# Kernel optimization log

Measured on AMD Instinct MI355X. Metric: run time of the kernel, lower is better.

## Reference

```python
import jax, jax.numpy as jnp
import numpy as np

N_NODES = 100000
N_EDGES = 1600000
D_IN = 64
D_HID = 64
D_ACT = 16


def gcn_conv(x, W, b, src, dst, n_nodes):
    """PyG-style GCNConv: D^-1/2 (A+I) D^-1/2 (x @ W) + b."""
    h = x @ W  # [N, out]
    ones = jnp.ones(src.shape[0], dtype=x.dtype)
    # degree with self-loops (in-degree + 1)
    deg = jax.ops.segment_sum(ones, dst, num_segments=n_nodes) + 1.0
    dinv = jax.lax.rsqrt(deg)  # [N]
    coef = dinv[src] * dinv[dst]  # [E]
    agg = jax.ops.segment_sum(h[src] * coef[:, None], dst, num_segments=n_nodes)
    agg = agg + h * (dinv * dinv)[:, None]  # self-loop term
    return agg + b


def setup_inputs() -> dict:
    key = jax.random.key(0)
    ks = jax.random.split(key, 6)
    x = jax.random.normal(ks[0], (N_NODES, D_IN), dtype=jnp.float32)
    edge_index = jax.random.randint(ks[1], (2, N_EDGES), 0, N_NODES, dtype=jnp.int64)
    s1 = 1.0 / np.sqrt(D_IN)
    s2 = 1.0 / np.sqrt(D_HID)
    W1 = jax.random.normal(ks[2], (D_IN, D_HID), dtype=jnp.float32) * s1
    b1 = jnp.zeros((D_HID,), dtype=jnp.float32)
    W2 = jax.random.normal(ks[3], (D_HID, D_HID), dtype=jnp.float32) * s2
    b2 = jnp.zeros((D_HID,), dtype=jnp.float32)
    Wfc = jax.random.normal(ks[4], (D_HID, D_ACT), dtype=jnp.float32) * s2
    bfc = jnp.zeros((D_ACT,), dtype=jnp.float32)
    return {"x": x, "edge_index": edge_index, "W1": W1, "b1": b1,
            "W2": W2, "b2": b2, "Wfc": Wfc, "bfc": bfc}


def reference(x, edge_index, W1, b1, W2, b2, Wfc, bfc):
    src, dst = edge_index[0], edge_index[1]
    n = x.shape[0]
    h = jax.nn.relu(gcn_conv(x, W1, b1, src, dst, n))
    h = jax.nn.relu(gcn_conv(h, W2, b2, src, dst, n))
    q_values = h @ Wfc + bfc
    return q_values
```

## Files before the change

kernel.cpp:

```cpp
#include <hip/hip_runtime.h>

#define NN 100000
#define NE 1600000
#define NCAP 64
#define NB2 782
#define NBP2 1024
#define CAPG 384
#define CHUNK 2048
#define NCHUNK 782

typedef __attribute__((ext_vector_type(8))) short short8;
typedef __attribute__((ext_vector_type(4))) float f32x4;

static __device__ __forceinline__ unsigned short f2bf(float f) {
    unsigned u = __float_as_uint(f);
    u += 0x7fffu + ((u >> 16) & 1u);
    return (unsigned short)(u >> 16);
}
static __device__ __forceinline__ float bflo(unsigned u) { return __uint_as_float(u << 16); }
static __device__ __forceinline__ float bfhi(unsigned u) { return __uint_as_float(u & 0xffff0000u); }

static __device__ __forceinline__ short8 as_s8(uint4 u) {
    union { uint4 u4; short8 s8; } x; x.u4 = u; return x.s8;
}
static __device__ __forceinline__ f32x4 mfma16(short8 a, short8 b, f32x4 c) {
    return __builtin_amdgcn_mfma_f32_16x16x32_bf16(a, b, c, 0, 0, 0);
}

static __device__ __forceinline__ void split8(float4 a, float4 b, short8& hi8, short8& lo8) {
    float vv[8] = {a.x, a.y, a.z, a.w, b.x, b.y, b.z, b.w};
    unsigned h[8], l[8];
    #pragma unroll
    for (int j = 0; j < 8; ++j) {
        h[j] = f2bf(vv[j]);
        l[j] = f2bf(vv[j] - bflo(h[j]));
    }
    uint4 uh, ul;
    uh.x = h[0] | (h[1] << 16); uh.y = h[2] | (h[3] << 16);
    uh.z = h[4] | (h[5] << 16); uh.w = h[6] | (h[7] << 16);
    ul.x = l[0] | (l[1] << 16); ul.y = l[2] | (l[3] << 16);
    ul.z = l[4] | (l[5] << 16); ul.w = l[6] | (l[7] << 16);
    hi8 = as_s8(uh); lo8 = as_s8(ul);
}

__global__ __launch_bounds__(256) void bin_edges(const int* __restrict__ src,
                                                 const int* __restrict__ dst,
                                                 int* __restrict__ gcur,
                                                 int* __restrict__ pairs) {
    __shared__ int lcnt[NBP2];
    __shared__ int lnext[NBP2];
    int t = threadIdx.x;
    int grp = blockIdx.x & 7;
    #pragma unroll
    for (int i = 0; i < 4; ++i) lcnt[t + 256 * i] = 0;
    __syncthreads();
    int base = blockIdx.x * CHUNK;
    int sr[8], dr[8];
    #pragma unroll
    for (int i = 0; i < 8; ++i) {
        int e = base + t + 256 * i;
        bool v = e < NE;
        sr[i] = v ? src[e] : 0;
        dr[i] = v ? dst[e] : -1;
        if (v) atomicAdd(&lcnt[dr[i] >> 7], 1);
    }
    __syncthreads();
    #pragma unroll
    for (int i = 0; i < 4; ++i) {
        int b = t + 256 * i;
        int v = lcnt[b];
        if (v) lnext[b] = ((grp << 10) + b) * CAPG + atomicAdd(&gcur[(grp << 10) + b], v);
    }
    __syncthreads();
    #pragma unroll
    for (int i = 0; i < 8; ++i) {
        if (dr[i] >= 0) {
            int p = atomicAdd(&lnext[dr[i] >> 7], 1);
            pairs[p] = sr[i] | ((dr[i] & 127) << 17);
        }
    }
}

__global__ __launch_bounds__(256) void slab_place(const int* __restrict__ pairs,
                                                  const int* __restrict__ gcur,
                                                  int* __restrict__ esrc,
                                                  int* __restrict__ cnt,
                                                  float* __restrict__ dinv) {
    __shared__ int lc[128];
    int b = blockIdx.x;
    int t = threadIdx.x;
    if (t < 128) lc[t] = 0;
    __syncthreads();
    #pragma unroll
    for (int g = 0; g < 8; ++g) {
        int rid = (g << 10) + b;
        int e0 = rid * CAPG;
        int n = min(gcur[rid], CAPG);
        for (int i = t; i < n; i += 256) {
            int w = pairs[e0 + i];
            int li = w >> 17;
            int p = atomicAdd(&lc[li], 1);
            if (p < NCAP - 1) esrc[(((b << 7) + li) << 6) + p] = w & 0x1FFFF;
        }
    }
    __syncthreads();
    if (t < 128) {
        int node = (b << 7) + t;
        if (node < NN) {
            int c = lc[t];
            int cc = min(c, NCAP - 1);
            esrc[(node << 6) + cc] = node;
            cnt[node] = cc + 1;
            dinv[node] = rsqrtf((float)c + 1.0f);
        }
    }
}

__global__ void wpack(const float* __restrict__ W1, const float* __restrict__ W2,
                      uint4* __restrict__ P, int* __restrict__ gcur) {
    int tid = blockIdx.x * blockDim.x + threadIdx.x;
    if (tid >= 1024) return;
    #pragma unroll
    for (int k = 0; k < 8; ++k) gcur[tid + 1024 * k] = 0;
    int w = tid >> 9;
    int f = tid & 511;
    int c = f >> 7;
    int t = (f >> 6) & 1;
    int lane = f & 63;
    const float* W = w ? W2 : W1;
    int k0 = t * 32 + (lane >> 4) * 8;
    int n  = c * 16 + (lane & 15);
    unsigned sh[8], sl[8];
    #pragma unroll
    for (int j = 0; j < 8; ++j) {
        float v = W[(k0 + j) * 64 + n];
        sh[j] = f2bf(v);
        sl[j] = f2bf(v - bflo(sh[j]));
    }
    uint4 ph, pl;
    ph.x = sh[0] | (sh[1] << 16); ph.y = sh[2] | (sh[3] << 16);
    ph.z = sh[4] | (sh[5] << 16); ph.w = sh[6] | (sh[7] << 16);
    pl.x = sl[0] | (sl[1] << 16); pl.y = sl[2] | (sl[3] << 16);
    pl.z = sl[4] | (sl[5] << 16); pl.w = sl[6] | (sl[7] << 16);
    P[w * 1024 + f]       = ph;
    P[w * 1024 + 512 + f] = pl;
}

__global__ __launch_bounds__(256) void gemm1_mfma(const float* __restrict__ X,
                                                  const uint4* __restrict__ WP,
                                                  const float* __restrict__ dinv,
                                                  uint4* __restrict__ G4) {
    __shared__ __align__(16) unsigned short Ls[4][16][64];
    int wave = threadIdx.x >> 6, lane = threadIdx.x & 63;
    int tile = blockIdx.x * 4 + wave;
    bool active = tile < (NN / 16);
    int node0 = (active ? tile : 0) * 16;
    int r = lane & 15, g = lane >> 4;

    const float* xr = X + (size_t)(node0 + r) * 64 + g * 8;
    float4 x0a = *(const float4*)(xr);
    float4 x0b = *(const float4*)(xr + 4);
    float4 x1a = *(const float4*)(xr + 32);
    float4 x1b = *(const float4*)(xr + 36);
    short8 ah0, al0, ah1, al1;
    split8(x0a, x0b, ah0, al0);
    split8(x1a, x1b, ah1, al1);

    f32x4 acc[4];
    #pragma unroll
    for (int c = 0; c < 4; ++c) acc[c] = (f32x4){0.f, 0.f, 0.f, 0.f};
    #pragma unroll
    for (int c = 0; c < 4; ++c) {
        short8 bh0 = as_s8(WP[(c * 2 + 0) * 64 + lane]);
        short8 bl0 = as_s8(WP[512 + (c * 2 + 0) * 64 + lane]);
        short8 bh1 = as_s8(WP[(c * 2 + 1) * 64 + lane]);
        short8 bl1 = as_s8(WP[512 + (c * 2 + 1) * 64 + lane]);
        acc[c] = mfma16(ah0, bh0, acc[c]);
        acc[c] = mfma16(al0, bh0, acc[c]);
        acc[c] = mfma16(ah0, bl0, acc[c]);
        acc[c] = mfma16(ah1, bh1, acc[c]);
        acc[c] = mfma16(al1, bh1, acc[c]);
        acc[c] = mfma16(ah1, bl1, acc[c]);
    }
    float dd[4];
    #pragma unroll
    for (int rr = 0; rr < 4; ++rr) dd[rr] = dinv[node0 + g * 4 + rr];
    #pragma unroll
    for (int c = 0; c < 4; ++c) {
        #pragma unroll
        for (int rr = 0; rr < 4; ++rr)
            Ls[wave][g * 4 + rr][c * 16 + r] = f2bf(acc[c][rr] * dd[rr]);
    }
    __syncthreads();
    if (active) {
        #pragma unroll
        for (int i = 0; i < 2; ++i) {
            int idx = lane + i * 64;
            int row = idx >> 3, u = idx & 7;
            G4[(size_t)(node0 + row) * 8 + u] = *(const uint4*)&Ls[wave][row][u * 8];
        }
    }
}

__global__ __launch_bounds__(256) void gemm2_mfma(const uint4* __restrict__ X4,
                                                  const uint4* __restrict__ WP,
                                                  const float* __restrict__ dinv,
                                                  uint4* __restrict__ G4) {
    __shared__ __align__(16) unsigned short Ls[4][16][64];
    int wave = threadIdx.x >> 6, lane = threadIdx.x & 63;
    int tile = blockIdx.x * 4 + wave;
    bool active = tile < (NN / 16);
    int node0 = (active ? tile : 0) * 16;
    int r = lane & 15, g = lane >> 4;

    short8 a0 = as_s8(X4[(size_t)(node0 + r) * 8 + g]);
    short8 a1 = as_s8(X4[(size_t)(node0 + r) * 8 + 4 + g]);

    f32x4 acc[4];
    #pragma unroll
    for (int c = 0; c < 4; ++c) acc[c] = (f32x4){0.f, 0.f, 0.f, 0.f};
    #pragma unroll
    for (int c = 0; c < 4; ++c) {
        short8 bh0 = as_s8(WP[(c * 2 + 0) * 64 + lane]);
        short8 bl0 = as_s8(WP[512 + (c * 2 + 0) * 64 + lane]);
        short8 bh1 = as_s8(WP[(c * 2 + 1) * 64 + lane]);
        short8 bl1 = as_s8(WP[512 + (c * 2 + 1) * 64 + lane]);
        acc[c] = mfma16(a0, bh0, acc[c]);
        acc[c] = mfma16(a0, bl0, acc[c]);
        acc[c] = mfma16(a1, bh1, acc[c]);
        acc[c] = mfma16(a1, bl1, acc[c]);
    }
    float dd[4];
    #pragma unroll
    for (int rr = 0; rr < 4; ++rr) dd[rr] = dinv[node0 + g * 4 + rr];
    #pragma unroll
    for (int c = 0; c < 4; ++c) {
        #pragma unroll
        for (int rr = 0; rr < 4; ++rr)
            Ls[wave][g * 4 + rr][c * 16 + r] = f2bf(acc[c][rr] * dd[rr]);
    }
    __syncthreads();
    if (active) {
        #pragma unroll
        for (int i = 0; i < 2; ++i) {
            int idx = lane + i * 64;
            int row = idx >> 3, u = idx & 7;
            G4[(size_t)(node0 + row) * 8 + u] = *(const uint4*)&Ls[wave][row][u * 8];
        }
    }
}

#define ACC8(u) do { \
    a0 += bflo((u).x); a1 += bfhi((u).x); a2 += bflo((u).y); a3 += bfhi((u).y); \
    a4 += bflo((u).z); a5 += bfhi((u).z); a6 += bflo((u).w); a7 += bfhi(u.w); } while (0)

#define GATHER_CORE(node)                                                     \
    int j0 = (node) << 6;                                                     \
    int e1 = j0 + cnt[node];                                                  \
    float a0 = 0.f, a1 = 0.f, a2 = 0.f, a3 = 0.f,                             \
          a4 = 0.f, a5 = 0.f, a6 = 0.f, a7 = 0.f;                             \
    int j = j0 + e;                                                           \
    for (; j + 8 < e1; j += 16) {                                             \
        int s0 = esrc[j], s1 = esrc[j + 8];                                   \
        uint4 u0 = G4[s0 * 8 + m];                                            \
        uint4 u1 = G4[s1 * 8 + m];                                            \
        ACC8(u0); ACC8(u1);                                                   \
    }                                                                         \
    for (; j < e1; j += 8) {                                                  \
        uint4 u = G4[esrc[j] * 8 + m];                                        \
        ACC8(u);                                                              \
    }                                                                         \
    a0 += __shfl_xor(a0, 8);  a1 += __shfl_xor(a1, 8);                        \
    a2 += __shfl_xor(a2, 8);  a3 += __shfl_xor(a3, 8);                        \
    a4 += __shfl_xor(a4, 8);  a5 += __shfl_xor(a5, 8);                        \
    a6 += __shfl_xor(a6, 8);  a7 += __shfl_xor(a7, 8);                        \
    a0 += __shfl_xor(a0, 16); a1 += __shfl_xor(a1, 16);                       \
    a2 += __shfl_xor(a2, 16); a3 += __shfl_xor(a3, 16);                       \
    a4 += __shfl_xor(a4, 16); a5 += __shfl_xor(a5, 16);                       \
    a6 += __shfl_xor(a6, 16); a7 += __shfl_xor(a7, 16);                       \
    a0 += __shfl_xor(a0, 32); a1 += __shfl_xor(a1, 32);                       \
    a2 += __shfl_xor(a2, 32); a3 += __shfl_xor(a3, 32);                       \
    a4 += __shfl_xor(a4, 32); a5 += __shfl_xor(a5, 32);                       \
    a6 += __shfl_xor(a6, 32); a7 += __shfl_xor(a7, 32);

__global__ __launch_bounds__(256) void gather_bf16(
        const int* __restrict__ cnt, const int* __restrict__ esrc,
        const float* __restrict__ dinv, const uint4* __restrict__ G4,
        const float* __restrict__ b, uint4* __restrict__ outH) {
    int node = blockIdx.x * 4 + (threadIdx.x >> 6);
    int lane = threadIdx.x & 63;
    int e = lane >> 3, m = lane & 7;
    GATHER_CORE(node)
    if (e == 0) {
        float dd = dinv[node];
        float4 b0 = ((const float4*)b)[2 * m];
        float4 b1v = ((const float4*)b)[2 * m + 1];
        float h0 = fmaxf(fmaf(a0, dd, b0.x), 0.f);
        float h1 = fmaxf(fmaf(a1, dd, b0.y), 0.f);
        float h2 = fmaxf(fmaf(a2, dd, b0.z), 0.f);
        float h3 = fmaxf(fmaf(a3, dd, b0.w), 0.f);
        float h4 = fmaxf(fmaf(a4, dd, b1v.x), 0.f);
        float h5 = fmaxf(fmaf(a5, dd, b1v.y), 0.f);
        float h6 = fmaxf(fmaf(a6, dd, b1v.z), 0.f);
        float h7 = fmaxf(fmaf(a7, dd, b1v.w), 0.f);
        uint4 pk;
        pk.x = (unsigned)f2bf(h0) | ((unsigned)f2bf(h1) << 16);
        pk.y = (unsigned)f2bf(h2) | ((unsigned)f2bf(h3) << 16);
        pk.z = (unsigned)f2bf(h4) | ((unsigned)f2bf(h5) << 16);
        pk.w = (unsigned)f2bf(h6) | ((unsigned)f2bf(h7) << 16);
        outH[(size_t)node * 8 + m] = pk;
    }
}

__global__ __launch_bounds__(256) void gather_fc(
        const int* __restrict__ cnt, const int* __restrict__ esrc,
        const float* __restrict__ dinv, const uint4* __restrict__ G4,
        const float* __restrict__ b2, const float* __restrict__ Wfc,
        const float* __restrict__ bfc, float* __restrict__ out) {
    int node = blockIdx.x * 4 + (threadIdx.x >> 6);
    int lane = threadIdx.x & 63;
    int e = lane >> 3, m = lane & 7;
    int q = lane >> 4, c = lane & 15;
    float Wreg[16];
    #pragma unroll
    for (int i = 0; i < 16; ++i) Wreg[i] = Wfc[(q * 16 + i) * 16 + c];
    GATHER_CORE(node)
    float dd = dinv[node];
    float4 b0 = ((const float4*)b2)[2 * m];
    float4 b1v = ((const float4*)b2)[2 * m + 1];
    a0 = fmaxf(fmaf(a0, dd, b0.x), 0.f);
    a1 = fmaxf(fmaf(a1, dd, b0.y), 0.f);
    a2 = fmaxf(fmaf(a2, dd, b0.z), 0.f);
    a3 = fmaxf(fmaf(a3, dd, b0.w), 0.f);
    a4 = fmaxf(fmaf(a4, dd, b1v.x), 0.f);
    a5 = fmaxf(fmaf(a5, dd, b1v.y), 0.f);
    a6 = fmaxf(fmaf(a6, dd, b1v.z), 0.f);
    a7 = fmaxf(fmaf(a7, dd, b1v.w), 0.f);
    int sl0 = 2 * q, sl1 = 2 * q + 1;
    float acc = 0.f;
    acc = fmaf(__shfl(a0, sl0), Wreg[0], acc);
    acc = fmaf(__shfl(a1, sl0), Wreg[1], acc);
    acc = fmaf(__shfl(a2, sl0), Wreg[2], acc);
    acc = fmaf(__shfl(a3, sl0), Wreg[3], acc);
    acc = fmaf(__shfl(a4, sl0), Wreg[4], acc);
    acc = fmaf(__shfl(a5, sl0), Wreg[5], acc);
    acc = fmaf(__shfl(a6, sl0), Wreg[6], acc);
    acc = fmaf(__shfl(a7, sl0), Wreg[7], acc);
    acc = fmaf(__shfl(a0, sl1), Wreg[8], acc);
    acc = fmaf(__shfl(a1, sl1), Wreg[9], acc);
    acc = fmaf(__shfl(a2, sl1), Wreg[10], acc);
    acc = fmaf(__shfl(a3, sl1), Wreg[11], acc);
    acc = fmaf(__shfl(a4, sl1), Wreg[12], acc);
    acc = fmaf(__shfl(a5, sl1), Wreg[13], acc);
    acc = fmaf(__shfl(a6, sl1), Wreg[14], acc);
    acc = fmaf(__shfl(a7, sl1), Wreg[15], acc);
    acc += __shfl_xor(acc, 16);
    acc += __shfl_xor(acc, 32);
    if (lane < 16) out[node * 16 + c] = acc + bfc[c];
}

extern "C" void kernel_launch(void* const* d_in, const int* in_sizes, int n_in,
                              void* d_out, int out_size, void* d_ws, size_t ws_size,
                              hipStream_t stream) {
    const float* x   = (const float*)d_in[0];
    const int*   ei  = (const int*)d_in[1];
    const float* W1  = (const float*)d_in[2];
    const float* b1  = (const float*)d_in[3];
    const float* W2  = (const float*)d_in[4];
    const float* b2  = (const float*)d_in[5];
    const float* Wfc = (const float*)d_in[6];
    const float* bfc = (const float*)d_in[7];
    float* out = (float*)d_out;

    const int* src = ei;
    const int* dst = ei + NE;

    int*      gcur  = (int*)d_ws;
    int*      cnt   = gcur + 8192;
    float*    dinvp = (float*)(cnt + NN);
    int*      esrc  = (int*)(dinvp + NN);
    unsigned* G     = (unsigned*)(esrc + (size_t)NN * NCAP);
    uint4*    bufB  = (uint4*)(G + (size_t)NN * 32);
    uint4*    WPK   = (uint4*)((unsigned*)bufB + (size_t)NN * 32);
    int*      pairs = (int*)bufB;

    wpack<<<4, 256, 0, stream>>>(W1, W2, WPK, gcur);
    bin_edges<<<NCHUNK, 256, 0, stream>>>(src, dst, gcur, pairs);
    slab_place<<<NB2, 256, 0, stream>>>(pairs, gcur, esrc, cnt, dinvp);

    gemm1_mfma<<<(NN / 16 + 3) / 4, 256, 0, stream>>>(x, WPK, dinvp, (uint4*)G);
    gather_bf16<<<NN / 4, 256, 0, stream>>>(cnt, esrc, dinvp, (const uint4*)G, b1, bufB);

    gemm2_mfma<<<(NN / 16 + 3) / 4, 256, 0, stream>>>(bufB, WPK + 1024, dinvp, (uint4*)G);
    gather_fc<<<NN / 4, 256, 0, stream>>>(cnt, esrc, dinvp, (const uint4*)G, b2, Wfc, bfc, out);
}
```

Baseline: 228.5 us.

## Fuse second-layer GEMM into first gather kernel via per-node MFMA

Removes the separate gemm2 kernel. Each wave that aggregates one node in the first gather now also multiplies the resulting hidden row by W2 using MFMA, with the row placed in lane r==0 of a 16-row tile and the other rows zeroed. It then writes the dinv-scaled bf16 G2 row directly. This saves a kernel launch and a full write and read of the intermediate hidden buffer. In exchange each wave issues 16 MFMAs and reloads the W2 fragments for a single useful row, so 15/16 of the matrix work is wasted.

```diff
diff --git a/kernel.cpp b/kernel.cpp
--- a/kernel.cpp
+++ b/kernel.cpp
@@ -202,57 +202,9 @@
     }
 }
 
-__global__ __launch_bounds__(256) void gemm2_mfma(const uint4* __restrict__ X4,
-                                                  const uint4* __restrict__ WP,
-                                                  const float* __restrict__ dinv,
-                                                  uint4* __restrict__ G4) {
-    __shared__ __align__(16) unsigned short Ls[4][16][64];
-    int wave = threadIdx.x >> 6, lane = threadIdx.x & 63;
-    int tile = blockIdx.x * 4 + wave;
-    bool active = tile < (NN / 16);
-    int node0 = (active ? tile : 0) * 16;
-    int r = lane & 15, g = lane >> 4;
-
-    short8 a0 = as_s8(X4[(size_t)(node0 + r) * 8 + g]);
-    short8 a1 = as_s8(X4[(size_t)(node0 + r) * 8 + 4 + g]);
-
-    f32x4 acc[4];
-    #pragma unroll
-    for (int c = 0; c < 4; ++c) acc[c] = (f32x4){0.f, 0.f, 0.f, 0.f};
-    #pragma unroll
-    for (int c = 0; c < 4; ++c) {
-        short8 bh0 = as_s8(WP[(c * 2 + 0) * 64 + lane]);
-        short8 bl0 = as_s8(WP[512 + (c * 2 + 0) * 64 + lane]);
-        short8 bh1 = as_s8(WP[(c * 2 + 1) * 64 + lane]);
-        short8 bl1 = as_s8(WP[512 + (c * 2 + 1) * 64 + lane]);
-        acc[c] = mfma16(a0, bh0, acc[c]);
-        acc[c] = mfma16(a0, bl0, acc[c]);
-        acc[c] = mfma16(a1, bh1, acc[c]);
-        acc[c] = mfma16(a1, bl1, acc[c]);
-    }
-    float dd[4];
-    #pragma unroll
-    for (int rr = 0; rr < 4; ++rr) dd[rr] = dinv[node0 + g * 4 + rr];
-    #pragma unroll
-    for (int c = 0; c < 4; ++c) {
-        #pragma unroll
-        for (int rr = 0; rr < 4; ++rr)
-            Ls[wave][g * 4 + rr][c * 16 + r] = f2bf(acc[c][rr] * dd[rr]);
-    }
-    __syncthreads();
-    if (active) {
-        #pragma unroll
-        for (int i = 0; i < 2; ++i) {
-            int idx = lane + i * 64;
-            int row = idx >> 3, u = idx & 7;
-            G4[(size_t)(node0 + row) * 8 + u] = *(const uint4*)&Ls[wave][row][u * 8];
-        }
-    }
-}
-
 #define ACC8(u) do { \
     a0 += bflo((u).x); a1 += bfhi((u).x); a2 += bflo((u).y); a3 += bfhi((u).y); \
-    a4 += bflo((u).z); a5 += bfhi((u).z); a6 += bflo((u).w); a7 += bfhi(u.w); } while (0)
+    a4 += bflo((u).z); a5 += bfhi((u).z); a6 += bflo((u).w); a7 += bfhi((u).w); } while (0)
 
 #define GATHER_CORE(node)                                                     \
     int j0 = (node) << 6;                                                     \
@@ -283,32 +235,76 @@
     a4 += __shfl_xor(a4, 32); a5 += __shfl_xor(a5, 32);                       \
     a6 += __shfl_xor(a6, 32); a7 += __shfl_xor(a7, 32);
 
-__global__ __launch_bounds__(256) void gather_bf16(
+__global__ __launch_bounds__(256) void gather_g2(
         const int* __restrict__ cnt, const int* __restrict__ esrc,
         const float* __restrict__ dinv, const uint4* __restrict__ G4,
-        const float* __restrict__ b, uint4* __restrict__ outH) {
-    int node = blockIdx.x * 4 + (threadIdx.x >> 6);
+        const float* __restrict__ b, const uint4* __restrict__ WP2,
+        uint4* __restrict__ G2) {
+    __shared__ float Ls[4][64];
+    int wave = threadIdx.x >> 6;
+    int node = blockIdx.x * 4 + wave;
     int lane = threadIdx.x & 63;
     int e = lane >> 3, m = lane & 7;
     GATHER_CORE(node)
-    if (e == 0) {
-        float dd = dinv[node];
-        float4 b0 = ((const float4*)b)[2 * m];
-        float4 b1v = ((const float4*)b)[2 * m + 1];
-        float h0 = fmaxf(fmaf(a0, dd, b0.x), 0.f);
-        float h1 = fmaxf(fmaf(a1, dd, b0.y), 0.f);
-        float h2 = fmaxf(fmaf(a2, dd, b0.z), 0.f);
-        float h3 = fmaxf(fmaf(a3, dd, b0.w), 0.f);
-        float h4 = fmaxf(fmaf(a4, dd, b1v.x), 0.f);
-        float h5 = fmaxf(fmaf(a5, dd, b1v.y), 0.f);
-        float h6 = fmaxf(fmaf(a6, dd, b1v.z), 0.f);
-        float h7 = fmaxf(fmaf(a7, dd, b1v.w), 0.f);
+    float dd = dinv[node];
+    float4 b0 = ((const float4*)b)[2 * m];
+    float4 b1v = ((const float4*)b)[2 * m + 1];
+    float h0 = fmaxf(fmaf(a0, dd, b0.x), 0.f);
+    float h1 = fmaxf(fmaf(a1, dd, b0.y), 0.f);
+    float h2 = fmaxf(fmaf(a2, dd, b0.z), 0.f);
+    float h3 = fmaxf(fmaf(a3, dd, b0.w), 0.f);
+    float h4 = fmaxf(fmaf(a4, dd, b1v.x), 0.f);
+    float h5 = fmaxf(fmaf(a5, dd, b1v.y), 0.f);
+    float h6 = fmaxf(fmaf(a6, dd, b1v.z), 0.f);
+    float h7 = fmaxf(fmaf(a7, dd, b1v.w), 0.f);
+    int r = lane & 15, g = lane >> 4;
+    bool live = (r == 0);
+    float t00 = __shfl(h0, g),     t01 = __shfl(h1, g),     t02 = __shfl(h2, g),     t03 = __shfl(h3, g);
+    float t04 = __shfl(h4, g),     t05 = __shfl(h5, g),     t06 = __shfl(h6, g),     t07 = __shfl(h7, g);
+    float t10 = __shfl(h0, 4 + g), t11 = __shfl(h1, 4 + g), t12 = __shfl(h2, 4 + g), t13 = __shfl(h3, 4 + g);
+    float t14 = __shfl(h4, 4 + g), t15 = __shfl(h5, 4 + g), t16 = __shfl(h6, 4 + g), t17 = __shfl(h7, 4 + g);
+    uint4 pk0, pk1;
+    if (live) {
+        pk0.x = (unsigned)f2bf(t00) | ((unsigned)f2bf(t01) << 16);
+        pk0.y = (unsigned)f2bf(t02) | ((unsigned)f2bf(t03) << 16);
+        pk0.z = (unsigned)f2bf(t04) | ((unsigned)f2bf(t05) << 16);
+        pk0.w = (unsigned)f2bf(t06) | ((unsigned)f2bf(t07) << 16);
+        pk1.x = (unsigned)f2bf(t10) | ((unsigned)f2bf(t11) << 16);
+        pk1.y = (unsigned)f2bf(t12) | ((unsigned)f2bf(t13) << 16);
+        pk1.z = (unsigned)f2bf(t14) | ((unsigned)f2bf(t15) << 16);
+        pk1.w = (unsigned)f2bf(t16) | ((unsigned)f2bf(t17) << 16);
+    } else {
+        pk0 = make_uint4(0, 0, 0, 0);
+        pk1 = make_uint4(0, 0, 0, 0);
+    }
+    short8 pa0 = as_s8(pk0), pa1 = as_s8(pk1);
+    float g2v[4];
+    #pragma unroll
+    for (int c = 0; c < 4; ++c) {
+        short8 bh0 = as_s8(WP2[(c * 2 + 0) * 64 + lane]);
+        short8 bl0 = as_s8(WP2[512 + (c * 2 + 0) * 64 + lane]);
+        short8 bh1 = as_s8(WP2[(c * 2 + 1) * 64 + lane]);
+        short8 bl1 = as_s8(WP2[512 + (c * 2 + 1) * 64 + lane]);
+        f32x4 t4 = (f32x4){0.f, 0.f, 0.f, 0.f};
+        t4 = mfma16(pa0, bh0, t4);
+        t4 = mfma16(pa0, bl0, t4);
+        t4 = mfma16(pa1, bh1, t4);
+        t4 = mfma16(pa1, bl1, t4);
+        g2v[c] = t4[0];
+    }
+    if (lane < 16) {
+        #pragma unroll
+        for (int c = 0; c < 4; ++c) Ls[wave][c * 16 + lane] = g2v[c] * dd;
+    }
+    if (lane < 8) {
+        float4 va = *(const float4*)&Ls[wave][8 * lane];
+        float4 vb = *(const float4*)&Ls[wave][8 * lane + 4];
         uint4 pk;
-        pk.x = (unsigned)f2bf(h0) | ((unsigned)f2bf(h1) << 16);
-        pk.y = (unsigned)f2bf(h2) | ((unsigned)f2bf(h3) << 16);
-        pk.z = (unsigned)f2bf(h4) | ((unsigned)f2bf(h5) << 16);
-        pk.w = (unsigned)f2bf(h6) | ((unsigned)f2bf(h7) << 16);
-        outH[(size_t)node * 8 + m] = pk;
+        pk.x = (unsigned)f2bf(va.x) | ((unsigned)f2bf(va.y) << 16);
+        pk.y = (unsigned)f2bf(va.z) | ((unsigned)f2bf(va.w) << 16);
+        pk.z = (unsigned)f2bf(vb.x) | ((unsigned)f2bf(vb.y) << 16);
+        pk.w = (unsigned)f2bf(vb.z) | ((unsigned)f2bf(vb.w) << 16);
+        G2[(size_t)node * 8 + lane] = pk;
     }
 }
 
@@ -380,17 +376,17 @@
     float*    dinvp = (float*)(cnt + NN);
     int*      esrc  = (int*)(dinvp + NN);
     unsigned* G     = (unsigned*)(esrc + (size_t)NN * NCAP);
-    uint4*    bufB  = (uint4*)(G + (size_t)NN * 32);
-    uint4*    WPK   = (uint4*)((unsigned*)bufB + (size_t)NN * 32);
-    int*      pairs = (int*)bufB;
+    uint4*    G2    = (uint4*)(G + (size_t)NN * 32);
+    uint4*    WPK   = (uint4*)((unsigned*)G2 + (size_t)NN * 32);
+    int*      pairs = (int*)G2;
 
     wpack<<<4, 256, 0, stream>>>(W1, W2, WPK, gcur);
     bin_edges<<<NCHUNK, 256, 0, stream>>>(src, dst, gcur, pairs);
     slab_place<<<NB2, 256, 0, stream>>>(pairs, gcur, esrc, cnt, dinvp);
 
     gemm1_mfma<<<(NN / 16 + 3) / 4, 256, 0, stream>>>(x, WPK, dinvp, (uint4*)G);
-    gather_bf16<<<NN / 4, 256, 0, stream>>>(cnt, esrc, dinvp, (const uint4*)G, b1, bufB);
-
-    gemm2_mfma<<<(NN / 16 + 3) / 4, 256, 0, stream>>>(bufB, WPK + 1024, dinvp, (uint4*)G);
-    gather_fc<<<NN / 4, 256, 0, stream>>>(cnt, esrc, dinvp, (const uint4*)G, b2, Wfc, bfc, out);
-}
+    gather_g2<<<NN / 4, 256, 0, stream>>>(cnt, esrc, dinvp, (const uint4*)G, b1,
+                                          WPK + 1024, G2);
+
+    gather_fc<<<NN / 4, 256, 0, stream>>>(cnt, esrc, dinvp, (const uint4*)G2, b2, Wfc, bfc, out);
+}
```

After: 251.8 us. 10.2% more time.

## Fuse edge slab placement with first-layer GEMM into one kernel

Applied to the files above, without the earlier changes.

Merges slab_place and gemm1_mfma into a single kernel. Each block places edges for its 128 nodes, computes dinv into shared memory, then runs the MFMA GEMM for those same 128 nodes. This removes one kernel launch and the global dinv reload. The pair reads are also widened to int4 vector loads, and the __syncthreads before the per-wave store in gemm2 is dropped because each wave only reads its own LDS tile. In exchange, the GEMM work now depends on per-block atomic placement finishing, which may serialize the two phases within a block.

```diff
diff --git a/kernel.cpp b/kernel.cpp
--- a/kernel.cpp
+++ b/kernel.cpp
@@ -81,12 +81,17 @@
     }
 }
 
-__global__ __launch_bounds__(256) void slab_place(const int* __restrict__ pairs,
+__global__ __launch_bounds__(256) void slab_gemm1(const int* __restrict__ pairs,
                                                   const int* __restrict__ gcur,
+                                                  const float* __restrict__ X,
+                                                  const uint4* __restrict__ WP,
                                                   int* __restrict__ esrc,
                                                   int* __restrict__ cnt,
-                                                  float* __restrict__ dinv) {
+                                                  float* __restrict__ dinv,
+                                                  uint4* __restrict__ G4) {
     __shared__ int lc[128];
+    __shared__ float ldv[128];
+    __shared__ __align__(16) unsigned short Ls[4][16][64];
     int b = blockIdx.x;
     int t = threadIdx.x;
     if (t < 128) lc[t] = 0;
@@ -96,11 +101,18 @@
         int rid = (g << 10) + b;
         int e0 = rid * CAPG;
         int n = min(gcur[rid], CAPG);
-        for (int i = t; i < n; i += 256) {
-            int w = pairs[e0 + i];
-            int li = w >> 17;
-            int p = atomicAdd(&lc[li], 1);
-            if (p < NCAP - 1) esrc[(((b << 7) + li) << 6) + p] = w & 0x1FFFF;
+        for (int i0 = t * 4; i0 < n; i0 += 1024) {
+            int4 w4 = *(const int4*)&pairs[e0 + i0];
+            int wv[4] = {w4.x, w4.y, w4.z, w4.w};
+            #pragma unroll
+            for (int k = 0; k < 4; ++k) {
+                if (i0 + k < n) {
+                    int w = wv[k];
+                    int li = w >> 17;
+                    int p = atomicAdd(&lc[li], 1);
+                    if (p < NCAP - 1) esrc[(((b << 7) + li) << 6) + p] = w & 0x1FFFF;
+                }
+            }
         }
     }
     __syncthreads();
@@ -111,7 +123,59 @@
             int cc = min(c, NCAP - 1);
             esrc[(node << 6) + cc] = node;
             cnt[node] = cc + 1;
-            dinv[node] = rsqrtf((float)c + 1.0f);
+            float dv = rsqrtf((float)c + 1.0f);
+            dinv[node] = dv;
+            ldv[t] = dv;
+        }
+    }
+    __syncthreads();
+
+    int wave = t >> 6, lane = t & 63;
+    int r = lane & 15, g = lane >> 4;
+    #pragma unroll
+    for (int ti = 0; ti < 2; ++ti) {
+        int T = wave * 2 + ti;
+        int node0 = (b << 7) + T * 16;
+        if (node0 < NN) {
+            const float* xr = X + (size_t)(node0 + r) * 64 + g * 8;
+            float4 x0a = *(const float4*)(xr);
+            float4 x0b = *(const float4*)(xr + 4);
+            float4 x1a = *(const float4*)(xr + 32);
+            float4 x1b = *(const float4*)(xr + 36);
+            short8 ah0, al0, ah1, al1;
+            split8(x0a, x0b, ah0, al0);
+            split8(x1a, x1b, ah1, al1);
+            f32x4 acc[4];
+            #pragma unroll
+            for (int c = 0; c < 4; ++c) acc[c] = (f32x4){0.f, 0.f, 0.f, 0.f};
+            #pragma unroll
+            for (int c = 0; c < 4; ++c) {
+                short8 bh0 = as_s8(WP[(c * 2 + 0) * 64 + lane]);
+                short8 bl0 = as_s8(WP[512 + (c * 2 + 0) * 64 + lane]);
+                short8 bh1 = as_s8(WP[(c * 2 + 1) * 64 + lane]);
+                short8 bl1 = as_s8(WP[512 + (c * 2 + 1) * 64 + lane]);
+                acc[c] = mfma16(ah0, bh0, acc[c]);
+                acc[c] = mfma16(al0, bh0, acc[c]);
+                acc[c] = mfma16(ah0, bl0, acc[c]);
+                acc[c] = mfma16(ah1, bh1, acc[c]);
+                acc[c] = mfma16(al1, bh1, acc[c]);
+                acc[c] = mfma16(ah1, bl1, acc[c]);
+            }
+            float dd[4];
+            #pragma unroll
+            for (int rr = 0; rr < 4; ++rr) dd[rr] = ldv[T * 16 + g * 4 + rr];
+            #pragma unroll
+            for (int c = 0; c < 4; ++c) {
+                #pragma unroll
+                for (int rr = 0; rr < 4; ++rr)
+                    Ls[wave][g * 4 + rr][c * 16 + r] = f2bf(acc[c][rr] * dd[rr]);
+            }
+            #pragma unroll
+            for (int i = 0; i < 2; ++i) {
+                int idx = lane + i * 64;
+                int row = idx >> 3, u = idx & 7;
+                G4[(size_t)(node0 + row) * 8 + u] = *(const uint4*)&Ls[wave][row][u * 8];
+            }
         }
     }
 }
@@ -146,62 +210,6 @@
     P[w * 1024 + 512 + f] = pl;
 }
 
-__global__ __launch_bounds__(256) void gemm1_mfma(const float* __restrict__ X,
-                                                  const uint4* __restrict__ WP,
-                                                  const float* __restrict__ dinv,
-                                                  uint4* __restrict__ G4) {
-    __shared__ __align__(16) unsigned short Ls[4][16][64];
-    int wave = threadIdx.x >> 6, lane = threadIdx.x & 63;
-    int tile = blockIdx.x * 4 + wave;
-    bool active = tile < (NN / 16);
-    int node0 = (active ? tile : 0) * 16;
-    int r = lane & 15, g = lane >> 4;
-
-    const float* xr = X + (size_t)(node0 + r) * 64 + g * 8;
-    float4 x0a = *(const float4*)(xr);
-    float4 x0b = *(const float4*)(xr + 4);
-    float4 x1a = *(const float4*)(xr + 32);
-    float4 x1b = *(const float4*)(xr + 36);
-    short8 ah0, al0, ah1, al1;
-    split8(x0a, x0b, ah0, al0);
-    split8(x1a, x1b, ah1, al1);
-
-    f32x4 acc[4];
-    #pragma unroll
-    for (int c = 0; c < 4; ++c) acc[c] = (f32x4){0.f, 0.f, 0.f, 0.f};
-    #pragma unroll
-    for (int c = 0; c < 4; ++c) {
-        short8 bh0 = as_s8(WP[(c * 2 + 0) * 64 + lane]);
-        short8 bl0 = as_s8(WP[512 + (c * 2 + 0) * 64 + lane]);
-        short8 bh1 = as_s8(WP[(c * 2 + 1) * 64 + lane]);
-        short8 bl1 = as_s8(WP[512 + (c * 2 + 1) * 64 + lane]);
-        acc[c] = mfma16(ah0, bh0, acc[c]);
-        acc[c] = mfma16(al0, bh0, acc[c]);
-        acc[c] = mfma16(ah0, bl0, acc[c]);
-        acc[c] = mfma16(ah1, bh1, acc[c]);
-        acc[c] = mfma16(al1, bh1, acc[c]);
-        acc[c] = mfma16(ah1, bl1, acc[c]);
-    }
-    float dd[4];
-    #pragma unroll
-    for (int rr = 0; rr < 4; ++rr) dd[rr] = dinv[node0 + g * 4 + rr];
-    #pragma unroll
-    for (int c = 0; c < 4; ++c) {
-        #pragma unroll
-        for (int rr = 0; rr < 4; ++rr)
-            Ls[wave][g * 4 + rr][c * 16 + r] = f2bf(acc[c][rr] * dd[rr]);
-    }
-    __syncthreads();
-    if (active) {
-        #pragma unroll
-        for (int i = 0; i < 2; ++i) {
-            int idx = lane + i * 64;
-            int row = idx >> 3, u = idx & 7;
-            G4[(size_t)(node0 + row) * 8 + u] = *(const uint4*)&Ls[wave][row][u * 8];
-        }
-    }
-}
-
 __global__ __launch_bounds__(256) void gemm2_mfma(const uint4* __restrict__ X4,
                                                   const uint4* __restrict__ WP,
                                                   const float* __restrict__ dinv,
@@ -239,7 +247,6 @@
         for (int rr = 0; rr < 4; ++rr)
             Ls[wave][g * 4 + rr][c * 16 + r] = f2bf(acc[c][rr] * dd[rr]);
     }
-    __syncthreads();
     if (active) {
         #pragma unroll
         for (int i = 0; i < 2; ++i) {
@@ -252,7 +259,7 @@
 
 #define ACC8(u) do { \
     a0 += bflo((u).x); a1 += bfhi((u).x); a2 += bflo((u).y); a3 += bfhi((u).y); \
-    a4 += bflo((u).z); a5 += bfhi((u).z); a6 += bflo((u).w); a7 += bfhi(u.w); } while (0)
+    a4 += bflo((u).z); a5 += bfhi((u).z); a6 += bflo((u).w); a7 += bfhi((u).w); } while (0)
 
 #define GATHER_CORE(node)                                                     \
     int j0 = (node) << 6;                                                     \
@@ -386,9 +393,8 @@
 
     wpack<<<4, 256, 0, stream>>>(W1, W2, WPK, gcur);
     bin_edges<<<NCHUNK, 256, 0, stream>>>(src, dst, gcur, pairs);
-    slab_place<<<NB2, 256, 0, stream>>>(pairs, gcur, esrc, cnt, dinvp);
-
-    gemm1_mfma<<<(NN / 16 + 3) / 4, 256, 0, stream>>>(x, WPK, dinvp, (uint4*)G);
+    slab_gemm1<<<NB2, 256, 0, stream>>>(pairs, gcur, x, WPK, esrc, cnt, dinvp, (uint4*)G);
+
     gather_bf16<<<NN / 4, 256, 0, stream>>>(cnt, esrc, dinvp, (const uint4*)G, b1, bufB);
 
     gemm2_mfma<<<(NN / 16 + 3) / 4, 256, 0, stream>>>(bufB, WPK + 1024, dinvp, (uint4*)G);
```

Result: no change. 226.3 us (median of 2 runs) (-1.0%).
